# Kernel optimization log

Hardware: AMD Instinct MI355X
Metric: run time of the kernel (lower is better)

Reference implementation:

```python
import jax, jax.numpy as jnp
import numpy as np

GAMMA = 0.99
NUM_QUANTILES = 50
STEP_TYPE_LAST = 2
HUBER_DELTA = 1.0

T, B, Q = 128, 512, NUM_QUANTILES


def setup_inputs() -> dict:
    key = jax.random.key(0)
    k1, k2, k3, k4, k5 = jax.random.split(key, 5)
    return {
        "reward": jax.random.normal(k1, (T, B), dtype=jnp.float32),
        "step_type": jax.random.randint(k2, (T, B), 0, 3, dtype=jnp.int32),
        "discount": jax.random.uniform(k3, (T, B), dtype=jnp.float32),
        "value": jax.random.normal(k4, (T, B, Q), dtype=jnp.float32),
        "target_value": jax.random.normal(k5, (T, B, Q), dtype=jnp.float32),
    }


def discounted_return(rewards, values, step_types, discounts):
    """alf value_ops.discounted_return: backward-in-time recurrence.

    rewards/step_types/discounts: [T, B]; values: [T, B, Q].
    Returns [T-1, B, Q]. rets[T-1]=values[T-1];
    rets[t] = is_last[t]*values[t] + (1-is_last[t])*(discounts[t+1]*rets[t+1] + rewards[t+1]).
    """
    is_last = (step_types == STEP_TYPE_LAST).astype(values.dtype)[..., None]  # [T,B,1]
    r = rewards[..., None]    # [T,B,1]
    d = discounts[..., None]  # [T,B,1]

    def step(carry, xs):
        is_last_t, v_t, r_tp1, d_tp1 = xs
        acc = carry * d_tp1 + r_tp1
        ret = is_last_t * v_t + (1.0 - is_last_t) * acc
        return ret, ret

    init = values[-1]
    xs = (is_last[:-1], values[:-1], r[1:], d[1:])
    _, rets = jax.lax.scan(step, init, xs, reverse=True)
    return rets  # [T-1, B, Q]


def huber(x):
    ax = jnp.abs(x)
    return jnp.where(ax <= HUBER_DELTA, 0.5 * x * x, HUBER_DELTA * (ax - 0.5 * HUBER_DELTA))


def reference(reward, step_type, discount, value, target_value):
    # td_lambda == 1.0 -> full discounted return (computed with no grad / detached)
    returns = jax.lax.stop_gradient(
        discounted_return(reward, target_value, step_type, discount * GAMMA))  # [T-1,B,Q]
    v = value[:-1]  # [T-1,B,Q]

    q = returns.shape[-1]
    tau = (jnp.arange(q, dtype=value.dtype) + 0.5) / q  # [Q] cdf midpoints

    # diff[..., i, j] = target_quantile_i - estimated_quantile_j
    diff = returns[..., :, None] - v[..., None, :]  # [T-1,B,Qt,Qe]
    weight = jnp.abs(tau - (jax.lax.stop_gradient(diff) < 0).astype(diff.dtype))
    loss = weight * huber(diff)
    # sum_over_quantiles=True: mean over target quantiles, sum over estimate quantiles
    loss = loss.mean(axis=-2).sum(axis=-1)  # [T-1,B]
    # tensor_extend_zero: append a zero row for the last time step -> [T,B]
    loss = jnp.concatenate([loss, jnp.zeros_like(loss[-1:])], axis=0)
    return loss
```

## Files before the change

### kernel.cpp

```cpp
#include <hip/hip_runtime.h>

#define GAMMA 0.99f
constexpr int T_DIM = 128;
constexpr int B_DIM = 512;
constexpr int Q_DIM = 50;
constexpr int TRET  = 127;
constexpr int SLOT  = 52;
constexpr int NPAIR = TRET * (Q_DIM/2);
constexpr int ASLOT = 64 * (Q_DIM/2);
constexpr int KEEP  = -1;

__global__ void __launch_bounds__(1024, 8) fused_kernel(
    const float* __restrict__ reward,
    const int*   __restrict__ step_type,
    const float* __restrict__ discount,
    const float* __restrict__ value,
    const float* __restrict__ tv,
    float*       __restrict__ out) {
  __shared__ __align__(16) float sret[TRET * SLOT];
  __shared__ __align__(16) float pacc[TRET * SLOT];
  __shared__ float s_alpha[TRET], s_beta[TRET];
  __shared__ int   s_anchor[TRET];

  const int tid = threadIdx.x;
  const int b   = blockIdx.x;

  const int  sa0 = tid,         sa1 = tid + 1024;
  const int  sb0 = 1600 + tid,  sb1 = 2624 + tid;
  const bool ha1 = (sa1 < ASLOT);
  const bool hb1 = (sb1 < NPAIR);

  auto vaddr = [&](int s) {
    const int t  = s / 25;
    const int j0 = (s - t * 25) * 2;
    return (t * B_DIM + b) * Q_DIM + j0;
  };
  float2 va0, va1, vb0, vb1;
  va0 = *reinterpret_cast<const float2*>(&value[vaddr(sa0)]);
  vb0 = *reinterpret_cast<const float2*>(&value[vaddr(sb0)]);
  if (ha1) va1 = *reinterpret_cast<const float2*>(&value[vaddr(sa1)]);
  if (hb1) vb1 = *reinterpret_cast<const float2*>(&value[vaddr(sb1)]);
  if (tid == 1023) out[TRET * B_DIM + b] = 0.0f;

  if (tid < 64) {
    const int t0 = tid, t1 = tid + 64;
    const bool  last0 = (step_type[t0 * B_DIM + b] == 2);
    const float d0    = GAMMA * discount[(t0 + 1) * B_DIM + b];
    const float r0    = reward[(t0 + 1) * B_DIM + b];
    float p0  = last0 ? 0.0f : d0;
    float qa0 = last0 ? 1.0f : 0.0f;
    float qb0 = last0 ? 0.0f : r0;
    int   nv0 = last0 ? t0   : KEEP;
    float p1 = 1.0f, qa1 = 0.0f, qb1 = 0.0f; int nv1 = KEEP;
    if (t1 < TRET) {
      const bool  last1 = (step_type[t1 * B_DIM + b] == 2);
      const float d1    = GAMMA * discount[(t1 + 1) * B_DIM + b];
      const float r1    = reward[(t1 + 1) * B_DIM + b];
      p1  = last1 ? 0.0f : d1;
      qa1 = last1 ? 1.0f : 0.0f;
      qb1 = last1 ? 0.0f : r1;
      nv1 = last1 ? t1   : KEEP;
    }
#pragma unroll
    for (int off = 1; off < 64; off <<= 1) {
      const int   src  = tid + off;
      const float xp0  = __shfl(p0,  src, 64), xp1  = __shfl(p1,  src, 64);
      const float xqa0 = __shfl(qa0, src, 64), xqa1 = __shfl(qa1, src, 64);
      const float xqb0 = __shfl(qb0, src, 64), xqb1 = __shfl(qb1, src, 64);
      const int   xnv0 = __shfl(nv0, src, 64), xnv1 = __shfl(nv1, src, 64);
      const bool  inl  = (src < 64);
      const float pp  = inl ? xp0  : xp1;
      const float pqa = inl ? xqa0 : xqa1;
      const float pqb = inl ? xqb0 : xqb1;
      const int   pnv = inl ? xnv0 : xnv1;
      qa0 = fmaf(p0, pqa, qa0);
      qb0 = fmaf(p0, pqb, qb0);
      p0  = p0 * pp;
      nv0 = (nv0 == KEEP) ? pnv : nv0;
      if (inl) {
        qa1 = fmaf(p1, xqa1, qa1);
        qb1 = fmaf(p1, xqb1, qb1);
        p1  = p1 * xp1;
        nv1 = (nv1 == KEEP) ? xnv1 : nv1;
      }
    }
    qa0 = fmaf(p0, qa1, qa0);
    qb0 = fmaf(p0, qb1, qb0);
    p0  = p0 * p1;
    nv0 = (nv0 == KEEP) ? nv1 : nv0;

    s_alpha[t0]  = p0 + qa0;
    s_beta[t0]   = qb0;
    s_anchor[t0] = (nv0 == KEEP) ? TRET : nv0;
    if (t1 < TRET) {
      s_alpha[t1]  = p1 + qa1;
      s_beta[t1]   = qb1;
      s_anchor[t1] = (nv1 == KEEP) ? TRET : nv1;
    }
  }
  __syncthreads();

  int bt0, bi0, bt1 = 0, bi1 = 0;
  float bA0, bB0, bA1 = 0.0f, bB1 = 0.0f;
  float2 btv0, btv1;
  {
    bt0 = sb0 / 25; bi0 = (sb0 - bt0 * 25) * 2;
    bA0 = s_alpha[bt0]; bB0 = s_beta[bt0];
    btv0 = *reinterpret_cast<const float2*>(
        &tv[(s_anchor[bt0] * B_DIM + b) * Q_DIM + bi0]);
  }
  if (hb1) {
    bt1 = sb1 / 25; bi1 = (sb1 - bt1 * 25) * 2;
    bA1 = s_alpha[bt1]; bB1 = s_beta[bt1];
    btv1 = *reinterpret_cast<const float2*>(
        &tv[(s_anchor[bt1] * B_DIM + b) * Q_DIM + bi1]);
  }

  auto stage = [&](int e) {
    const int t = e / 25;
    const int i = (e - t * 25) * 2;
    const float a  = s_alpha[t];
    const float be = s_beta[t];
    const float2 tvv = *reinterpret_cast<const float2*>(
        &tv[(s_anchor[t] * B_DIM + b) * Q_DIM + i]);
    *reinterpret_cast<float2*>(&sret[t * SLOT + i]) =
        make_float2(fmaf(a, tvv.x, be), fmaf(a, tvv.y, be));
  };
  stage(sa0);
  if (ha1) stage(sa1);
  __syncthreads();

  auto compute_slot = [&](int s, float2 vv) {
    const int t  = s / 25;
    const int j0 = (s - t * 25) * 2;
    const float ta0 = ((float)j0 + 0.5f) * (1.0f / Q_DIM) - 0.5f;
    const float ta1 = ((float)j0 + 1.5f) * (1.0f / Q_DIM) - 0.5f;
    const float* rp = &sret[t * SLOT];
    float s1a = 0.0f, s2a = 0.0f, s1b = 0.0f, s2b = 0.0f;
    auto pair2 = [&](float reti) {
      { const float d = reti - vv.x;
        const float c = __builtin_amdgcn_fmed3f(d, -1.0f, 1.0f);
        const float e = fmaf(-0.5f, c, d);
        s1a = fmaf(e, c, s1a);
        s2a = fmaf(e, fabsf(c), s2a); }
      { const float d = reti - vv.y;
        const float c = __builtin_amdgcn_fmed3f(d, -1.0f, 1.0f);
        const float e = fmaf(-0.5f, c, d);
        s1b = fmaf(e, c, s1b);
        s2b = fmaf(e, fabsf(c), s2b); }
    };
#pragma unroll
    for (int i0 = 0; i0 < 48; i0 += 4) {
      const float4 rr = *reinterpret_cast<const float4*>(rp + i0);
      pair2(rr.x); pair2(rr.y); pair2(rr.z); pair2(rr.w);
    }
    {
      const float2 rr = *reinterpret_cast<const float2*>(rp + 48);
      pair2(rr.x); pair2(rr.y);
    }
    *reinterpret_cast<float2*>(&pacc[t * SLOT + j0]) =
        make_float2(fmaf(ta0, s2a, 0.5f * s1a), fmaf(ta1, s2b, 0.5f * s1b));
  };

  compute_slot(sa0, va0);
  if (ha1) compute_slot(sa1, va1);

  *reinterpret_cast<float2*>(&sret[bt0 * SLOT + bi0]) =
      make_float2(fmaf(bA0, btv0.x, bB0), fmaf(bA0, btv0.y, bB0));
  if (hb1)
    *reinterpret_cast<float2*>(&sret[bt1 * SLOT + bi1]) =
        make_float2(fmaf(bA1, btv1.x, bB1), fmaf(bA1, btv1.y, bB1));
  __syncthreads();

  compute_slot(sb0, vb0);
  if (hb1) compute_slot(sb1, vb1);
  __syncthreads();

  const int w    = tid >> 6;
  const int lane = tid & 63;
#pragma unroll
  for (int k = 0; k < 8; ++k) {
    const int t = w * 8 + k;
    if (t < TRET) {
      float x = (lane < Q_DIM) ? pacc[t * SLOT + lane] : 0.0f;
#pragma unroll
      for (int off = 32; off > 0; off >>= 1)
        x += __shfl_xor(x, off, 64);
      if (lane == 0) out[t * B_DIM + b] = x * (1.0f / Q_DIM);
    }
  }
}

extern "C" void kernel_launch(void* const* d_in, const int* in_sizes, int n_in,
                              void* d_out, int out_size, void* d_ws, size_t ws_size,
                              hipStream_t stream) {
  const float* reward       = (const float*)d_in[0];
  const int*   step_type    = (const int*)  d_in[1];
  const float* discount     = (const float*)d_in[2];
  const float* value        = (const float*)d_in[3];
  const float* target_value = (const float*)d_in[4];
  float* out = (float*)d_out;

  fused_kernel<<<B_DIM, 1024, 0, stream>>>(reward, step_type, discount,
                                           value, target_value, out);
}
```

Baseline: 107.0 us.

## Stage all returns at once and drop two-phase compute pipeline

Replaces the two-phase scheme, where half the returns were staged, computed on, then the rest staged, with a single phase. Each thread now loads four target-value and value pairs, writes all returns to shared memory, syncs once, and runs four compute slots. This removes one barrier and simplifies the indexing, but it also drops the overlap of the second half's global loads with the first half's compute. It also keeps more loads in flight per thread, which raises register pressure.

```diff
diff --git a/kernel.cpp b/kernel.cpp
--- a/kernel.cpp
+++ b/kernel.cpp
@@ -7,7 +7,6 @@
 constexpr int TRET  = 127;
 constexpr int SLOT  = 52;
 constexpr int NPAIR = TRET * (Q_DIM/2);
-constexpr int ASLOT = 64 * (Q_DIM/2);
 constexpr int KEEP  = -1;
 
 __global__ void __launch_bounds__(1024, 8) fused_kernel(
@@ -25,21 +24,6 @@
   const int tid = threadIdx.x;
   const int b   = blockIdx.x;
 
-  const int  sa0 = tid,         sa1 = tid + 1024;
-  const int  sb0 = 1600 + tid,  sb1 = 2624 + tid;
-  const bool ha1 = (sa1 < ASLOT);
-  const bool hb1 = (sb1 < NPAIR);
-
-  auto vaddr = [&](int s) {
-    const int t  = s / 25;
-    const int j0 = (s - t * 25) * 2;
-    return (t * B_DIM + b) * Q_DIM + j0;
-  };
-  float2 va0, va1, vb0, vb1;
-  va0 = *reinterpret_cast<const float2*>(&value[vaddr(sa0)]);
-  vb0 = *reinterpret_cast<const float2*>(&value[vaddr(sb0)]);
-  if (ha1) va1 = *reinterpret_cast<const float2*>(&value[vaddr(sa1)]);
-  if (hb1) vb1 = *reinterpret_cast<const float2*>(&value[vaddr(sb1)]);
   if (tid == 1023) out[TRET * B_DIM + b] = 0.0f;
 
   if (tid < 64) {
@@ -100,39 +84,45 @@
   }
   __syncthreads();
 
-  int bt0, bi0, bt1 = 0, bi1 = 0;
-  float bA0, bB0, bA1 = 0.0f, bB1 = 0.0f;
-  float2 btv0, btv1;
-  {
-    bt0 = sb0 / 25; bi0 = (sb0 - bt0 * 25) * 2;
-    bA0 = s_alpha[bt0]; bB0 = s_beta[bt0];
-    btv0 = *reinterpret_cast<const float2*>(
-        &tv[(s_anchor[bt0] * B_DIM + b) * Q_DIM + bi0]);
-  }
-  if (hb1) {
-    bt1 = sb1 / 25; bi1 = (sb1 - bt1 * 25) * 2;
-    bA1 = s_alpha[bt1]; bB1 = s_beta[bt1];
-    btv1 = *reinterpret_cast<const float2*>(
-        &tv[(s_anchor[bt1] * B_DIM + b) * Q_DIM + bi1]);
-  }
+  const int e0 = tid, e1 = tid + 1024, e2 = tid + 2048, e3 = tid + 3072;
+  const bool h3 = (e3 < NPAIR);
+  const int t0 = e0 / 25, i0 = (e0 - t0 * 25) * 2;
+  const int t1 = e1 / 25, i1 = (e1 - t1 * 25) * 2;
+  const int t2 = e2 / 25, i2 = (e2 - t2 * 25) * 2;
+  const int t3 = h3 ? e3 / 25 : 0;
+  const int i3 = h3 ? (e3 - t3 * 25) * 2 : 0;
 
-  auto stage = [&](int e) {
-    const int t = e / 25;
-    const int i = (e - t * 25) * 2;
-    const float a  = s_alpha[t];
-    const float be = s_beta[t];
-    const float2 tvv = *reinterpret_cast<const float2*>(
-        &tv[(s_anchor[t] * B_DIM + b) * Q_DIM + i]);
-    *reinterpret_cast<float2*>(&sret[t * SLOT + i]) =
-        make_float2(fmaf(a, tvv.x, be), fmaf(a, tvv.y, be));
-  };
-  stage(sa0);
-  if (ha1) stage(sa1);
+  const float A0 = s_alpha[t0], Be0 = s_beta[t0];
+  const float A1 = s_alpha[t1], Be1 = s_beta[t1];
+  const float A2 = s_alpha[t2], Be2 = s_beta[t2];
+  const float A3 = s_alpha[t3], Be3 = s_beta[t3];
+  const int   n0 = s_anchor[t0], n1 = s_anchor[t1];
+  const int   n2 = s_anchor[t2], n3 = s_anchor[t3];
+
+  const float2 g0 = *reinterpret_cast<const float2*>(&tv[(n0 * B_DIM + b) * Q_DIM + i0]);
+  const float2 g1 = *reinterpret_cast<const float2*>(&tv[(n1 * B_DIM + b) * Q_DIM + i1]);
+  const float2 g2 = *reinterpret_cast<const float2*>(&tv[(n2 * B_DIM + b) * Q_DIM + i2]);
+  float2 g3 = make_float2(0.f, 0.f);
+  if (h3) g3 = *reinterpret_cast<const float2*>(&tv[(n3 * B_DIM + b) * Q_DIM + i3]);
+
+  const float2 v0 = *reinterpret_cast<const float2*>(&value[(t0 * B_DIM + b) * Q_DIM + i0]);
+  const float2 v1 = *reinterpret_cast<const float2*>(&value[(t1 * B_DIM + b) * Q_DIM + i1]);
+  const float2 v2 = *reinterpret_cast<const float2*>(&value[(t2 * B_DIM + b) * Q_DIM + i2]);
+  float2 v3 = make_float2(0.f, 0.f);
+  if (h3) v3 = *reinterpret_cast<const float2*>(&value[(t3 * B_DIM + b) * Q_DIM + i3]);
+
+  *reinterpret_cast<float2*>(&sret[t0 * SLOT + i0]) =
+      make_float2(fmaf(A0, g0.x, Be0), fmaf(A0, g0.y, Be0));
+  *reinterpret_cast<float2*>(&sret[t1 * SLOT + i1]) =
+      make_float2(fmaf(A1, g1.x, Be1), fmaf(A1, g1.y, Be1));
+  *reinterpret_cast<float2*>(&sret[t2 * SLOT + i2]) =
+      make_float2(fmaf(A2, g2.x, Be2), fmaf(A2, g2.y, Be2));
+  if (h3)
+    *reinterpret_cast<float2*>(&sret[t3 * SLOT + i3]) =
+        make_float2(fmaf(A3, g3.x, Be3), fmaf(A3, g3.y, Be3));
   __syncthreads();
 
-  auto compute_slot = [&](int s, float2 vv) {
-    const int t  = s / 25;
-    const int j0 = (s - t * 25) * 2;
+  auto compute_slot = [&](int t, int j0, float2 vv) {
     const float ta0 = ((float)j0 + 0.5f) * (1.0f / Q_DIM) - 0.5f;
     const float ta1 = ((float)j0 + 1.5f) * (1.0f / Q_DIM) - 0.5f;
     const float* rp = &sret[t * SLOT];
@@ -150,8 +140,8 @@
         s2b = fmaf(e, fabsf(c), s2b); }
     };
 #pragma unroll
-    for (int i0 = 0; i0 < 48; i0 += 4) {
-      const float4 rr = *reinterpret_cast<const float4*>(rp + i0);
+    for (int k = 0; k < 48; k += 4) {
+      const float4 rr = *reinterpret_cast<const float4*>(rp + k);
       pair2(rr.x); pair2(rr.y); pair2(rr.z); pair2(rr.w);
     }
     {
@@ -162,18 +152,10 @@
         make_float2(fmaf(ta0, s2a, 0.5f * s1a), fmaf(ta1, s2b, 0.5f * s1b));
   };
 
-  compute_slot(sa0, va0);
-  if (ha1) compute_slot(sa1, va1);
-
-  *reinterpret_cast<float2*>(&sret[bt0 * SLOT + bi0]) =
-      make_float2(fmaf(bA0, btv0.x, bB0), fmaf(bA0, btv0.y, bB0));
-  if (hb1)
-    *reinterpret_cast<float2*>(&sret[bt1 * SLOT + bi1]) =
-        make_float2(fmaf(bA1, btv1.x, bB1), fmaf(bA1, btv1.y, bB1));
-  __syncthreads();
-
-  compute_slot(sb0, vb0);
-  if (hb1) compute_slot(sb1, vb1);
+  compute_slot(t0, i0, v0);
+  compute_slot(t1, i1, v1);
+  compute_slot(t2, i2, v2);
+  if (h3) compute_slot(t3, i3, v3);
   __syncthreads();
 
   const int w    = tid >> 6;
```

Result: no change. 105.7 us (-1.2%).
